# Kernel tuning notes

Measured on AMD Instinct MI355X. Metric: run time of the kernel, lower is better.

The kernel has to match this reference:

```python
import jax, jax.numpy as jnp
import numpy as np

B, L, N, H, D, TOPK = 32, 720, 512, 16, 64, 8
TEMP = 1.0


def setup_inputs() -> dict:
    key = jax.random.key(0)
    ks = jax.random.split(key, 18)
    s = lambda k, shp, fan: jax.random.normal(k, shp, jnp.float32) / np.sqrt(fan)
    return {
        'x': jax.random.normal(ks[0], (B, L, N), jnp.float32),
        'var_embed': s(ks[1], (N, H), H),
        'Wq': s(ks[2], (H, H), H), 'bq': jnp.zeros((H,), jnp.float32),
        'Wk': s(ks[3], (H, H), H), 'bk': jnp.zeros((H,), jnp.float32),
        'Wscore': s(ks[4], (N, 1), N), 'bscore': jnp.zeros((1,), jnp.float32),
        'Wc1': s(ks[5], (N, D), N), 'bc1': jnp.zeros((D,), jnp.float32),
        'Wc2': s(ks[6], (D, D), D), 'bc2': jnp.zeros((D,), jnp.float32),
        'Wcn': s(ks[7], (D, N), D), 'bcn': jnp.zeros((N,), jnp.float32),
        'Wg': s(ks[8], (2 * N, N), 2 * N), 'bg': jnp.zeros((N,), jnp.float32),
        'Wf': s(ks[9], (N, N), N), 'bf': jnp.zeros((N,), jnp.float32),
        'gamma': jnp.ones((N,), jnp.float32), 'beta': jnp.zeros((N,), jnp.float32),
    }


def _forward(x, var_embed, Wq, bq, Wk, bk, Wscore, bscore, Wc1, bc1, Wc2, bc2,
             Wcn, bcn, Wg, bg, Wf, bf, gamma, beta):
    # --- SparseVariableRouter (eval mode: no gumbel noise) ---
    Q = var_embed @ Wq + bq          # [N,H]
    K = var_embed @ Wk + bk          # [N,H]
    sim = Q @ K.T                    # [N,N] (identical across batch in torch)
    eye = jnp.eye(N, dtype=bool)
    sim = jnp.where(eye, -1e9, sim)
    topk_vals, topk_idx = jax.lax.top_k(sim, TOPK)      # [N,k]
    w = jax.nn.softmax(topk_vals / TEMP, axis=-1)        # [N,k]
    x_perm = jnp.transpose(x, (0, 2, 1))                 # [B,N,L]
    neighbors = x_perm[:, topk_idx, :]                   # [B,N,k,L] gather
    ring_out = jnp.einsum('bnkl,nk->bln', neighbors, w)  # [B,L,N]
    # --- center path ---
    attn = jax.nn.softmax(x @ Wscore + bscore, axis=1)   # [B,L,1] softmax over L
    center_raw = jnp.sum(x * attn, axis=1)               # [B,N]
    c = jax.nn.gelu(center_raw @ Wc1 + bc1, approximate=False)
    c = jax.nn.gelu(c @ Wc2 + bc2, approximate=False)
    center = c @ Wcn + bcn                               # [B,N]
    center_b = jnp.broadcast_to(center[:, None, :], (x.shape[0], x.shape[1], N))
    # --- gated fusion + residual LN ---
    gate = jax.nn.sigmoid(jnp.concatenate([ring_out, center_b], axis=-1) @ Wg + bg)
    fused = gate * ring_out + (1.0 - gate) * center_b
    fused = fused @ Wf + bf
    h = fused + x
    mu = jnp.mean(h, axis=-1, keepdims=True)
    var = jnp.var(h, axis=-1, keepdims=True)
    return (h - mu) * jax.lax.rsqrt(var + 1e-5) * gamma + beta


def reference(x, var_embed, Wq, bq, Wk, bk, Wscore, bscore, Wc1, bc1, Wc2, bc2,
              Wcn, bcn, Wg, bg, Wf, bf, gamma, beta):
    return _forward(x, var_embed, Wq, bq, Wk, bk, Wscore, bscore, Wc1, bc1,
                    Wc2, bc2, Wcn, bcn, Wg, bg, Wf, bf, gamma, beta)
```

## Files before the change

### kernel.cpp

```cpp
#include <hip/hip_runtime.h>
#include <hip/hip_bf16.h>
#include <math.h>

#define B_ 32
#define L_ 720
#define N_ 512
#define H_ 16
#define D_ 64
#define TOPK_ 8
#define M_ (B_ * L_)
#define RPB 8
#define CRCH 16
#define CRL (L_ / CRCH)

typedef __bf16 bf16x8 __attribute__((ext_vector_type(8)));
typedef float f32x16 __attribute__((ext_vector_type(16)));

__device__ __forceinline__ void async_cp16(const __hip_bfloat16* g, __hip_bfloat16* l) {
    __builtin_amdgcn_global_load_lds(
        (const __attribute__((address_space(1))) void*)g,
        (__attribute__((address_space(3))) void*)l, 16, 0, 0);
}

__device__ __forceinline__ bf16x8 frag_ld(const __hip_bfloat16* base, int row, int j0) {
    return *(const bf16x8*)(base + row * 64 + (((j0) ^ (row & 7)) << 3));
}

__global__ __launch_bounds__(512) void qk_kernel(
    const float* __restrict__ ve,
    const float* __restrict__ Wq, const float* __restrict__ bq,
    const float* __restrict__ Wk, const float* __restrict__ bk,
    float* __restrict__ Qm, float* __restrict__ Km)
{
    const int g = blockIdx.x * 512 + threadIdx.x;
    const int j = g >> 4, h = g & 15;
    const float* vr = ve + j * H_;
    float q = bq[h], k = bk[h];
    #pragma unroll
    for (int m = 0; m < H_; ++m) {
        const float v = vr[m];
        q += v * Wq[m * H_ + h];
        k += v * Wk[m * H_ + h];
    }
    Qm[g] = q;
    Km[g] = k;
}

__global__ __launch_bounds__(64) void topk_kernel(
    const float* __restrict__ Qm, const float* __restrict__ Km,
    float* __restrict__ w_out, int* __restrict__ idx_out)
{
    const int n = blockIdx.x;
    const int lane = threadIdx.x;

    float4 q0, q1, q2, q3;
    {
        const float4* qr = (const float4*)(Qm + n * H_);
        q0 = qr[0]; q1 = qr[1]; q2 = qr[2]; q3 = qr[3];
    }

    float sv[8]; int si[8];
    #pragma unroll
    for (int c = 0; c < 8; ++c) {
        const int j = c * 64 + lane;
        const float4* kr = (const float4*)(Km + j * H_);
        float4 k0 = kr[0], k1 = kr[1], k2 = kr[2], k3 = kr[3];
        float s = q0.x * k0.x + q0.y * k0.y + q0.z * k0.z + q0.w * k0.w
                + q1.x * k1.x + q1.y * k1.y + q1.z * k1.z + q1.w * k1.w
                + q2.x * k2.x + q2.y * k2.y + q2.z * k2.z + q2.w * k2.w
                + q3.x * k3.x + q3.y * k3.y + q3.z * k3.z + q3.w * k3.w;
        sv[c] = (j == n) ? -1e9f : s;
        si[c] = j;
    }

    float keepv[TOPK_]; int keepi[TOPK_];
    #pragma unroll
    for (int k = 0; k < TOPK_; ++k) {
        float bv = sv[0]; int bi = si[0]; int bslot = 0;
        #pragma unroll
        for (int c = 1; c < 8; ++c)
            if (sv[c] > bv || (sv[c] == bv && si[c] < bi)) { bv = sv[c]; bi = si[c]; bslot = c; }
        float v = bv; int i = bi;
        #pragma unroll
        for (int off = 32; off > 0; off >>= 1) {
            float v2 = __shfl_xor(v, off);
            int   i2 = __shfl_xor(i, off);
            if (v2 > v || (v2 == v && i2 < i)) { v = v2; i = i2; }
        }
        keepv[k] = v; keepi[k] = i;
        if (i == bi) sv[bslot] = -INFINITY;
    }

    if (lane == 0) {
        float vmax = keepv[0];
        float ev[TOPK_], esum = 0.f;
        #pragma unroll
        for (int k = 0; k < TOPK_; k++) { ev[k] = expf(keepv[k] - vmax); esum += ev[k]; }
        float inv = 1.f / esum;
        #pragma unroll
        for (int k = 0; k < TOPK_; k++) {
            w_out[n * TOPK_ + k] = ev[k] * inv;
            idx_out[n * TOPK_ + k] = keepi[k];
        }
    }
}

__global__ __launch_bounds__(512) void ring_kernel(
    const float* __restrict__ x, const float* __restrict__ w,
    const int* __restrict__ idx,
    const float* __restrict__ Wscore, const float* __restrict__ bscore,
    __hip_bfloat16* __restrict__ ring, float* __restrict__ s)
{
    __shared__ float xs[RPB][N_];
    __shared__ float wsh[N_ * TOPK_];
    __shared__ int   ish[N_ * TOPK_];
    const int t = threadIdx.x;
    const int row0 = blockIdx.x * RPB;

    for (int i = t; i < N_ * TOPK_; i += 512) { wsh[i] = w[i]; ish[i] = idx[i]; }
    {
        const float4* xg = (const float4*)(x + (size_t)row0 * N_);
        float4* xsf = (float4*)&xs[0][0];
        xsf[t] = xg[t];
        xsf[t + 512] = xg[t + 512];
    }
    __syncthreads();

    {
        const int wv = t >> 6, lane = t & 63;
        float sa = 0.f;
        #pragma unroll
        for (int i = 0; i < 8; ++i) sa += xs[wv][lane + i * 64] * Wscore[lane + i * 64];
        for (int off = 32; off > 0; off >>= 1) sa += __shfl_down(sa, off);
        if (lane == 0) s[row0 + wv] = sa + bscore[0];
    }

    float wr[TOPK_]; int ir[TOPK_];
    #pragma unroll
    for (int k = 0; k < TOPK_; ++k) { wr[k] = wsh[t * TOPK_ + k]; ir[k] = ish[t * TOPK_ + k]; }
    #pragma unroll
    for (int r = 0; r < RPB; ++r) {
        float acc = 0.f;
        #pragma unroll
        for (int k = 0; k < TOPK_; ++k) acc += wr[k] * xs[r][ir[k]];
        ring[(size_t)(row0 + r) * N_ + t] = __float2bfloat16(acc);
    }
}

__global__ __launch_bounds__(256) void attn_softmax_kernel(float* __restrict__ s)
{
    const int b = blockIdx.x;
    const int t = threadIdx.x;
    float* row = s + (size_t)b * L_;

    __shared__ float sm[4];
    __shared__ float sm2[4];

    float lmax = -1e30f;
    for (int l = t; l < L_; l += 256) lmax = fmaxf(lmax, row[l]);
    for (int off = 32; off > 0; off >>= 1) lmax = fmaxf(lmax, __shfl_down(lmax, off));
    if ((t & 63) == 0) sm[t >> 6] = lmax;
    __syncthreads();
    float gmax = fmaxf(fmaxf(sm[0], sm[1]), fmaxf(sm[2], sm[3]));

    float lsum = 0.f;
    for (int l = t; l < L_; l += 256) {
        float e = expf(row[l] - gmax);
        row[l] = e;
        lsum += e;
    }
    for (int off = 32; off > 0; off >>= 1) lsum += __shfl_down(lsum, off);
    if ((t & 63) == 0) sm2[t >> 6] = lsum;
    __syncthreads();
    float inv = 1.f / (sm2[0] + sm2[1] + sm2[2] + sm2[3]);
    for (int l = t; l < L_; l += 256) row[l] *= inv;
}

__global__ __launch_bounds__(512) void center_raw_kernel(
    const float* __restrict__ x, const float* __restrict__ attn,
    float* __restrict__ craw_p)
{
    const int b = blockIdx.x >> 4;
    const int c = blockIdx.x & 15;
    const int n = threadIdx.x;
    __shared__ float ash[CRL];
    const int l0 = c * CRL;
    if (n < CRL) ash[n] = attn[b * L_ + l0 + n];
    __syncthreads();
    const float* xb = x + ((size_t)b * L_ + l0) * N_;
    float acc = 0.f;
    #pragma unroll 3
    for (int l = 0; l < CRL; l++) acc += ash[l] * xb[(size_t)l * N_ + n];
    craw_p[(size_t)(b * CRCH + c) * N_ + n] = acc;
}

__device__ __forceinline__ float gelu_exact(float v) {
    return 0.5f * v * (1.0f + erff(v * 0.70710678118654752440f));
}

__global__ __launch_bounds__(512) void center_mlp_kernel(
    const float* __restrict__ craw_p,
    const float* __restrict__ Wc1, const float* __restrict__ bc1,
    const float* __restrict__ Wc2, const float* __restrict__ bc2,
    const float* __restrict__ Wcn, const float* __restrict__ bcn,
    float* __restrict__ center)
{
    const int b = blockIdx.x;
    const int t = threadIdx.x;
    const int col = t & 63;
    const int seg = t >> 6;
    __shared__ float cr[N_];
    __shared__ float psum[8][D_];
    __shared__ float h1[D_];
    __shared__ float h2[D_];

    {
        float acc = 0.f;
        #pragma unroll
        for (int c = 0; c < CRCH; ++c) acc += craw_p[(size_t)(b * CRCH + c) * N_ + t];
        cr[t] = acc;
    }
    __syncthreads();
    {
        float p = 0.f;
        #pragma unroll 8
        for (int m = seg * 64; m < seg * 64 + 64; ++m) p += cr[m] * Wc1[m * D_ + col];
        psum[seg][col] = p;
    }
    __syncthreads();
    if (t < D_) {
        float acc = bc1[t];
        #pragma unroll
        for (int s2 = 0; s2 < 8; ++s2) acc += psum[s2][t];
        h1[t] = gelu_exact(acc);
    }
    __syncthreads();
    if (t < D_) {
        float acc = bc2[t];
        #pragma unroll 8
        for (int j = 0; j < D_; j++) acc += h1[j] * Wc2[j * D_ + t];
        h2[t] = gelu_exact(acc);
    }
    __syncthreads();
    {
        float acc = bcn[t];
        #pragma unroll 8
        for (int j = 0; j < D_; j++) acc += h2[j] * Wcn[j * N_ + t];
        center[b * N_ + t] = acc;
    }
}

__global__ __launch_bounds__(512) void cg_kernel(
    const float* __restrict__ center, const float* __restrict__ Wg,
    const float* __restrict__ bg, float* __restrict__ cg)
{
    const int nc = blockIdx.x;
    const int b  = blockIdx.y;
    const int t  = threadIdx.x;
    const int col = nc * 64 + (t & 63);
    const int seg = t >> 6;
    __shared__ float cs[N_];
    __shared__ float psum[8][64];

    cs[t] = center[b * N_ + t];
    __syncthreads();
    {
        float p = 0.f;
        const float* wp = Wg + (size_t)(N_ + seg * 64) * N_ + col;
        #pragma unroll 8
        for (int m = 0; m < 64; ++m) { p += cs[seg * 64 + m] * wp[0]; wp += N_; }
        psum[seg][t & 63] = p;
    }
    __syncthreads();
    if (t < 64) {
        float acc = bg[nc * 64 + t];
        #pragma unroll
        for (int s2 = 0; s2 < 8; ++s2) acc += psum[s2][t];
        cg[b * N_ + nc * 64 + t] = acc;
    }
}

__global__ __launch_bounds__(256) void convert_kernel(
    const float* __restrict__ Wg, const float* __restrict__ Wf,
    __hip_bfloat16* __restrict__ WgT, __hip_bfloat16* __restrict__ WfT)
{
    const int n = blockIdx.x & 511;
    const bool isf = blockIdx.x >= 512;
    const float* src = isf ? Wf : Wg;
    __hip_bfloat16* dst = isf ? WfT : WgT;
    for (int k = threadIdx.x; k < N_; k += 256)
        dst[n * N_ + k] = __float2bfloat16(src[(size_t)k * N_ + n]);
}

#define GEMM_BODY(EPILOGUE)                                                    \
    __shared__ __hip_bfloat16 Ash[128 * 64];                                   \
    __shared__ __hip_bfloat16 Bsh[128 * 64];                                   \
    const int tid  = threadIdx.x;                                              \
    const int lane = tid & 63;                                                 \
    const int wv   = tid >> 6;                                                 \
    const int m32  = lane & 31;                                                \
    const int half = lane >> 5;                                                \
    const int wr   = wv >> 1;                                                  \
    const int wc   = wv & 1;                                                   \
    const int row0 = blockIdx.x * 128;                                         \
    const int n0   = blockIdx.y * 128;                                         \
    const int swz  = (lane & 7) ^ (lane >> 3);                                 \
    const int rln  = lane >> 3;                                                \
    f32x16 acc[2][2];                                                          \
    _Pragma("unroll") for (int i = 0; i < 2; i++)                              \
        _Pragma("unroll") for (int j = 0; j < 2; j++)                          \
            _Pragma("unroll") for (int e = 0; e < 16; e++) acc[i][j][e] = 0.f; \
    for (int step = 0; step < 8; ++step) {                                     \
        const int k0 = step * 64;                                              \
        const __hip_bfloat16* Ab = A  + (size_t)row0 * N_ + k0 + swz * 8;      \
        const __hip_bfloat16* Bb = BT + (size_t)n0   * N_ + k0 + swz * 8;      \
        __syncthreads();                                                       \
        _Pragma("unroll") for (int j = 0; j < 4; ++j) {                        \
            const int r = j * 32 + wv * 8 + rln;                               \
            const int lb = (j * 256 + wv * 64) * 8;                            \
            async_cp16(Ab + (size_t)r * N_, Ash + lb);                         \
            async_cp16(Bb + (size_t)r * N_, Bsh + lb);                         \
        }                                                                      \
        __syncthreads();                                                       \
        _Pragma("unroll") for (int ks = 0; ks < 4; ++ks) {                     \
            const int j0 = ks * 2 + half;                                      \
            bf16x8 a0 = frag_ld(Ash, wr * 64      + m32, j0);                  \
            bf16x8 a1 = frag_ld(Ash, wr * 64 + 32 + m32, j0);                  \
            bf16x8 b0 = frag_ld(Bsh, wc * 64      + m32, j0);                  \
            bf16x8 b1 = frag_ld(Bsh, wc * 64 + 32 + m32, j0);                  \
            acc[0][0] = __builtin_amdgcn_mfma_f32_32x32x16_bf16(a0, b0, acc[0][0], 0, 0, 0); \
            acc[0][1] = __builtin_amdgcn_mfma_f32_32x32x16_bf16(a0, b1, acc[0][1], 0, 0, 0); \
            acc[1][0] = __builtin_amdgcn_mfma_f32_32x32x16_bf16(a1, b0, acc[1][0], 0, 0, 0); \
            acc[1][1] = __builtin_amdgcn_mfma_f32_32x32x16_bf16(a1, b1, acc[1][1], 0, 0, 0); \
        }                                                                      \
    }                                                                          \
    _Pragma("unroll") for (int mi = 0; mi < 2; ++mi)                           \
        _Pragma("unroll") for (int ni = 0; ni < 2; ++ni)                       \
            _Pragma("unroll") for (int reg = 0; reg < 16; ++reg) {             \
                const int rg  = row0 + wr * 64 + mi * 32 +                     \
                                (reg & 3) + 8 * (reg >> 2) + 4 * half;         \
                const int col = n0 + wc * 64 + ni * 32 + m32;                  \
                const float aval = acc[mi][ni][reg];                           \
                EPILOGUE                                                       \
            }

__global__ __launch_bounds__(256) void gemm_gate_kernel(
    const __hip_bfloat16* __restrict__ A,
    const __hip_bfloat16* __restrict__ BT,
    const float* __restrict__ cg,
    const float* __restrict__ center,
    __hip_bfloat16* __restrict__ fused)
{
    GEMM_BODY({
        const int b = rg / L_;
        const float logit = aval + cg[b * N_ + col];
        const float g = 1.f / (1.f + expf(-logit));
        const float rv = __bfloat162float(A[(size_t)rg * N_ + col]);
        const float f = g * rv + (1.f - g) * center[b * N_ + col];
        fused[(size_t)rg * N_ + col] = __float2bfloat16(f);
    })
}

__global__ __launch_bounds__(256) void gemm_out_kernel(
    const __hip_bfloat16* __restrict__ A,
    const __hip_bfloat16* __restrict__ BT,
    const float* __restrict__ x,
    const float* __restrict__ bfv,
    float* __restrict__ out)
{
    GEMM_BODY({
        out[(size_t)rg * N_ + col] = aval + bfv[col] + x[(size_t)rg * N_ + col];
    })
}

__global__ __launch_bounds__(512) void ln_kernel(
    float* __restrict__ out,
    const float* __restrict__ gamma, const float* __restrict__ beta)
{
    const int tid = threadIdx.x;
    const int r = tid >> 7;
    const int c = tid & 127;
    const int row = blockIdx.x * 4 + r;
    const int wid = tid >> 6;
    __shared__ float ls[8], lq[8];

    float4 v = ((const float4*)(out + (size_t)row * N_))[c];
    float sum = v.x + v.y + v.z + v.w;
    float sq  = v.x * v.x + v.y * v.y + v.z * v.z + v.w * v.w;
    for (int off = 32; off > 0; off >>= 1) {
        sum += __shfl_down(sum, off);
        sq  += __shfl_down(sq,  off);
    }
    if ((tid & 63) == 0) { ls[wid] = sum; lq[wid] = sq; }
    __syncthreads();
    const float S  = ls[2 * r] + ls[2 * r + 1];
    const float Q2 = lq[2 * r] + lq[2 * r + 1];
    const float mu  = S * (1.0f / N_);
    const float var = Q2 * (1.0f / N_) - mu * mu;
    const float inv = 1.0f / sqrtf(var + 1e-5f);
    const float4 g4 = ((const float4*)gamma)[c];
    const float4 b4 = ((const float4*)beta)[c];
    float4 o;
    o.x = (v.x - mu) * inv * g4.x + b4.x;
    o.y = (v.y - mu) * inv * g4.y + b4.y;
    o.z = (v.z - mu) * inv * g4.z + b4.z;
    o.w = (v.w - mu) * inv * g4.w + b4.w;
    ((float4*)(out + (size_t)row * N_))[c] = o;
}

extern "C" void kernel_launch(void* const* d_in, const int* in_sizes, int n_in,
                              void* d_out, int out_size, void* d_ws, size_t ws_size,
                              hipStream_t stream) {
    const float* x       = (const float*)d_in[0];
    const float* ve      = (const float*)d_in[1];
    const float* Wq      = (const float*)d_in[2];
    const float* bq      = (const float*)d_in[3];
    const float* Wk      = (const float*)d_in[4];
    const float* bk      = (const float*)d_in[5];
    const float* Wscore  = (const float*)d_in[6];
    const float* bscore  = (const float*)d_in[7];
    const float* Wc1     = (const float*)d_in[8];
    const float* bc1     = (const float*)d_in[9];
    const float* Wc2     = (const float*)d_in[10];
    const float* bc2     = (const float*)d_in[11];
    const float* Wcn     = (const float*)d_in[12];
    const float* bcn     = (const float*)d_in[13];
    const float* Wg      = (const float*)d_in[14];
    const float* bg      = (const float*)d_in[15];
    const float* Wf      = (const float*)d_in[16];
    const float* bf      = (const float*)d_in[17];
    const float* gamma   = (const float*)d_in[18];
    const float* beta    = (const float*)d_in[19];
    float* out = (float*)d_out;

    char* p = (char*)d_ws;
    float* ws_w    = (float*)p; p += N_ * TOPK_ * sizeof(float);
    int*   ws_idx  = (int*)p;   p += N_ * TOPK_ * sizeof(int);
    float* ws_s    = (float*)p; p += B_ * L_ * sizeof(float);
    float* ws_crp  = (float*)p; p += B_ * CRCH * N_ * sizeof(float);
    float* ws_cent = (float*)p; p += B_ * N_ * sizeof(float);
    float* ws_cg   = (float*)p; p += B_ * N_ * sizeof(float);
    float* ws_Q    = (float*)p; p += N_ * H_ * sizeof(float);
    float* ws_K    = (float*)p; p += N_ * H_ * sizeof(float);
    __hip_bfloat16* ws_ring  = (__hip_bfloat16*)p; p += (size_t)M_ * N_ * sizeof(__hip_bfloat16);
    __hip_bfloat16* ws_fused = (__hip_bfloat16*)p; p += (size_t)M_ * N_ * sizeof(__hip_bfloat16);
    __hip_bfloat16* ws_WgT   = (__hip_bfloat16*)p; p += (size_t)N_ * N_ * sizeof(__hip_bfloat16);
    __hip_bfloat16* ws_WfT   = (__hip_bfloat16*)p; p += (size_t)N_ * N_ * sizeof(__hip_bfloat16);

    convert_kernel<<<1024, 256, 0, stream>>>(Wg, Wf, ws_WgT, ws_WfT);
    qk_kernel<<<16, 512, 0, stream>>>(ve, Wq, bq, Wk, bk, ws_Q, ws_K);
    topk_kernel<<<N_, 64, 0, stream>>>(ws_Q, ws_K, ws_w, ws_idx);
    ring_kernel<<<M_ / RPB, 512, 0, stream>>>(x, ws_w, ws_idx, Wscore, bscore,
                                              ws_ring, ws_s);
    attn_softmax_kernel<<<B_, 256, 0, stream>>>(ws_s);
    center_raw_kernel<<<B_ * CRCH, 512, 0, stream>>>(x, ws_s, ws_crp);
    center_mlp_kernel<<<B_, 512, 0, stream>>>(ws_crp, Wc1, bc1, Wc2, bc2,
                                              Wcn, bcn, ws_cent);
    cg_kernel<<<dim3(8, B_), 512, 0, stream>>>(ws_cent, Wg, bg, ws_cg);
    dim3 ggrid(M_ / 128, N_ / 128);
    gemm_gate_kernel<<<ggrid, 256, 0, stream>>>(ws_ring, ws_WgT, ws_cg,
                                                ws_cent, ws_fused);
    gemm_out_kernel<<<ggrid, 256, 0, stream>>>(ws_fused, ws_WfT, x, bf, out);
    ln_kernel<<<M_ / 4, 512, 0, stream>>>(out, gamma, beta);
}
```

Baseline: 268.8 us.

## Fuse gate GEMM, output GEMM and LayerNorm into one row-tile kernel

```diff
diff --git a/kernel.cpp b/kernel.cpp
--- a/kernel.cpp
+++ b/kernel.cpp
@@ -12,6 +12,7 @@
 #define RPB 8
 #define CRCH 16
 #define CRL (L_ / CRCH)
+#define MT 64
 
 typedef __bf16 bf16x8 __attribute__((ext_vector_type(8)));
 typedef float f32x16 __attribute__((ext_vector_type(16)));
@@ -22,28 +23,39 @@
         (__attribute__((address_space(3))) void*)l, 16, 0, 0);
 }
 
-__device__ __forceinline__ bf16x8 frag_ld(const __hip_bfloat16* base, int row, int j0) {
-    return *(const bf16x8*)(base + row * 64 + (((j0) ^ (row & 7)) << 3));
-}
-
-__global__ __launch_bounds__(512) void qk_kernel(
+__device__ __forceinline__ int sw_idx(int row, int col) {
+    return row * 512 + (((col >> 3) ^ (row & 7)) << 3) + (col & 7);
+}
+
+__global__ __launch_bounds__(256) void prep_kernel(
+    const float* __restrict__ Wg, const float* __restrict__ Wf,
+    __hip_bfloat16* __restrict__ WgT, __hip_bfloat16* __restrict__ WfT,
     const float* __restrict__ ve,
     const float* __restrict__ Wq, const float* __restrict__ bq,
     const float* __restrict__ Wk, const float* __restrict__ bk,
     float* __restrict__ Qm, float* __restrict__ Km)
 {
-    const int g = blockIdx.x * 512 + threadIdx.x;
-    const int j = g >> 4, h = g & 15;
-    const float* vr = ve + j * H_;
-    float q = bq[h], k = bk[h];
-    #pragma unroll
-    for (int m = 0; m < H_; ++m) {
-        const float v = vr[m];
-        q += v * Wq[m * H_ + h];
-        k += v * Wk[m * H_ + h];
-    }
-    Qm[g] = q;
-    Km[g] = k;
+    if (blockIdx.x < 1024) {
+        const int n = blockIdx.x & 511;
+        const bool isf = blockIdx.x >= 512;
+        const float* src = isf ? Wf : Wg;
+        __hip_bfloat16* dst = isf ? WfT : WgT;
+        for (int k = threadIdx.x; k < N_; k += 256)
+            dst[n * N_ + k] = __float2bfloat16(src[(size_t)k * N_ + n]);
+    } else {
+        const int g = (blockIdx.x - 1024) * 256 + threadIdx.x;
+        const int j = g >> 4, h = g & 15;
+        const float* vr = ve + j * H_;
+        float q = bq[h], k = bk[h];
+        #pragma unroll
+        for (int m = 0; m < H_; ++m) {
+            const float v = vr[m];
+            q += v * Wq[m * H_ + h];
+            k += v * Wk[m * H_ + h];
+        }
+        Qm[g] = q;
+        Km[g] = k;
+    }
 }
 
 __global__ __launch_bounds__(64) void topk_kernel(
@@ -147,46 +159,40 @@
     }
 }
 
-__global__ __launch_bounds__(256) void attn_softmax_kernel(float* __restrict__ s)
-{
-    const int b = blockIdx.x;
-    const int t = threadIdx.x;
-    float* row = s + (size_t)b * L_;
-
-    __shared__ float sm[4];
-    __shared__ float sm2[4];
-
-    float lmax = -1e30f;
-    for (int l = t; l < L_; l += 256) lmax = fmaxf(lmax, row[l]);
-    for (int off = 32; off > 0; off >>= 1) lmax = fmaxf(lmax, __shfl_down(lmax, off));
-    if ((t & 63) == 0) sm[t >> 6] = lmax;
-    __syncthreads();
-    float gmax = fmaxf(fmaxf(sm[0], sm[1]), fmaxf(sm[2], sm[3]));
-
-    float lsum = 0.f;
-    for (int l = t; l < L_; l += 256) {
-        float e = expf(row[l] - gmax);
-        row[l] = e;
-        lsum += e;
-    }
-    for (int off = 32; off > 0; off >>= 1) lsum += __shfl_down(lsum, off);
-    if ((t & 63) == 0) sm2[t >> 6] = lsum;
-    __syncthreads();
-    float inv = 1.f / (sm2[0] + sm2[1] + sm2[2] + sm2[3]);
-    for (int l = t; l < L_; l += 256) row[l] *= inv;
-}
-
 __global__ __launch_bounds__(512) void center_raw_kernel(
-    const float* __restrict__ x, const float* __restrict__ attn,
+    const float* __restrict__ x, const float* __restrict__ s,
     float* __restrict__ craw_p)
 {
     const int b = blockIdx.x >> 4;
     const int c = blockIdx.x & 15;
     const int n = threadIdx.x;
+    __shared__ float red[8];
     __shared__ float ash[CRL];
+    const float* srow = s + (size_t)b * L_;
+
+    const float v1 = srow[n];
+    const float v2 = (n < L_ - 512) ? srow[512 + n] : -1e30f;
+    float lmax = fmaxf(v1, v2);
+    for (int off = 32; off > 0; off >>= 1) lmax = fmaxf(lmax, __shfl_xor(lmax, off));
+    if ((n & 63) == 0) red[n >> 6] = lmax;
+    __syncthreads();
+    float gmax = red[0];
+    #pragma unroll
+    for (int i = 1; i < 8; ++i) gmax = fmaxf(gmax, red[i]);
+    __syncthreads();
+    float lsum = expf(v1 - gmax) + ((n < L_ - 512) ? expf(v2 - gmax) : 0.f);
+    for (int off = 32; off > 0; off >>= 1) lsum += __shfl_xor(lsum, off);
+    if ((n & 63) == 0) red[n >> 6] = lsum;
+    __syncthreads();
+    float gsum = 0.f;
+    #pragma unroll
+    for (int i = 0; i < 8; ++i) gsum += red[i];
+    const float inv = 1.f / gsum;
+
     const int l0 = c * CRL;
-    if (n < CRL) ash[n] = attn[b * L_ + l0 + n];
-    __syncthreads();
+    if (n < CRL) ash[n] = expf(srow[l0 + n] - gmax) * inv;
+    __syncthreads();
+
     const float* xb = x + ((size_t)b * L_ + l0) * N_;
     float acc = 0.f;
     #pragma unroll 3
@@ -280,132 +286,137 @@
     }
 }
 
-__global__ __launch_bounds__(256) void convert_kernel(
-    const float* __restrict__ Wg, const float* __restrict__ Wf,
-    __hip_bfloat16* __restrict__ WgT, __hip_bfloat16* __restrict__ WfT)
-{
-    const int n = blockIdx.x & 511;
-    const bool isf = blockIdx.x >= 512;
-    const float* src = isf ? Wf : Wg;
-    __hip_bfloat16* dst = isf ? WfT : WgT;
-    for (int k = threadIdx.x; k < N_; k += 256)
-        dst[n * N_ + k] = __float2bfloat16(src[(size_t)k * N_ + n]);
-}
-
-#define GEMM_BODY(EPILOGUE)                                                    \
-    __shared__ __hip_bfloat16 Ash[128 * 64];                                   \
-    __shared__ __hip_bfloat16 Bsh[128 * 64];                                   \
-    const int tid  = threadIdx.x;                                              \
-    const int lane = tid & 63;                                                 \
-    const int wv   = tid >> 6;                                                 \
-    const int m32  = lane & 31;                                                \
-    const int half = lane >> 5;                                                \
-    const int wr   = wv >> 1;                                                  \
-    const int wc   = wv & 1;                                                   \
-    const int row0 = blockIdx.x * 128;                                         \
-    const int n0   = blockIdx.y * 128;                                         \
-    const int swz  = (lane & 7) ^ (lane >> 3);                                 \
-    const int rln  = lane >> 3;                                                \
-    f32x16 acc[2][2];                                                          \
-    _Pragma("unroll") for (int i = 0; i < 2; i++)                              \
-        _Pragma("unroll") for (int j = 0; j < 2; j++)                          \
-            _Pragma("unroll") for (int e = 0; e < 16; e++) acc[i][j][e] = 0.f; \
-    for (int step = 0; step < 8; ++step) {                                     \
-        const int k0 = step * 64;                                              \
-        const __hip_bfloat16* Ab = A  + (size_t)row0 * N_ + k0 + swz * 8;      \
-        const __hip_bfloat16* Bb = BT + (size_t)n0   * N_ + k0 + swz * 8;      \
-        __syncthreads();                                                       \
-        _Pragma("unroll") for (int j = 0; j < 4; ++j) {                        \
-            const int r = j * 32 + wv * 8 + rln;                               \
-            const int lb = (j * 256 + wv * 64) * 8;                            \
-            async_cp16(Ab + (size_t)r * N_, Ash + lb);                         \
-            async_cp16(Bb + (size_t)r * N_, Bsh + lb);                         \
+#define KLOOP(ATILE, BPTR, ACC)                                                \
+    _Pragma("unroll 4")                                                        \
+    for (int ks = 0; ks < 32; ++ks) {                                          \
+        const int arow = wr * 32 + m32;                                        \
+        bf16x8 a = *(const bf16x8*)(ATILE + arow * 512 +                       \
+                      (((2 * ks + half) ^ (arow & 7)) << 3));                  \
+        _Pragma("unroll")                                                      \
+        for (int ni = 0; ni < 4; ++ni) {                                       \
+            const int n = wc * 128 + ni * 32 + m32;                            \
+            bf16x8 b = *(const bf16x8*)(BPTR + (size_t)n * 512 +               \
+                                        ks * 16 + half * 8);                   \
+            ACC[ni] = __builtin_amdgcn_mfma_f32_32x32x16_bf16(a, b, ACC[ni], 0, 0, 0); \
         }                                                                      \
-        __syncthreads();                                                       \
-        _Pragma("unroll") for (int ks = 0; ks < 4; ++ks) {                     \
-            const int j0 = ks * 2 + half;                                      \
-            bf16x8 a0 = frag_ld(Ash, wr * 64      + m32, j0);                  \
-            bf16x8 a1 = frag_ld(Ash, wr * 64 + 32 + m32, j0);                  \
-            bf16x8 b0 = frag_ld(Bsh, wc * 64      + m32, j0);                  \
-            bf16x8 b1 = frag_ld(Bsh, wc * 64 + 32 + m32, j0);                  \
-            acc[0][0] = __builtin_amdgcn_mfma_f32_32x32x16_bf16(a0, b0, acc[0][0], 0, 0, 0); \
-            acc[0][1] = __builtin_amdgcn_mfma_f32_32x32x16_bf16(a0, b1, acc[0][1], 0, 0, 0); \
-            acc[1][0] = __builtin_amdgcn_mfma_f32_32x32x16_bf16(a1, b0, acc[1][0], 0, 0, 0); \
-            acc[1][1] = __builtin_amdgcn_mfma_f32_32x32x16_bf16(a1, b1, acc[1][1], 0, 0, 0); \
-        }                                                                      \
-    }                                                                          \
-    _Pragma("unroll") for (int mi = 0; mi < 2; ++mi)                           \
-        _Pragma("unroll") for (int ni = 0; ni < 2; ++ni)                       \
-            _Pragma("unroll") for (int reg = 0; reg < 16; ++reg) {             \
-                const int rg  = row0 + wr * 64 + mi * 32 +                     \
-                                (reg & 3) + 8 * (reg >> 2) + 4 * half;         \
-                const int col = n0 + wc * 64 + ni * 32 + m32;                  \
-                const float aval = acc[mi][ni][reg];                           \
-                EPILOGUE                                                       \
-            }
-
-__global__ __launch_bounds__(256) void gemm_gate_kernel(
-    const __hip_bfloat16* __restrict__ A,
-    const __hip_bfloat16* __restrict__ BT,
-    const float* __restrict__ cg,
-    const float* __restrict__ center,
-    __hip_bfloat16* __restrict__ fused)
-{
-    GEMM_BODY({
-        const int b = rg / L_;
-        const float logit = aval + cg[b * N_ + col];
-        const float g = 1.f / (1.f + expf(-logit));
-        const float rv = __bfloat162float(A[(size_t)rg * N_ + col]);
-        const float f = g * rv + (1.f - g) * center[b * N_ + col];
-        fused[(size_t)rg * N_ + col] = __float2bfloat16(f);
-    })
-}
-
-__global__ __launch_bounds__(256) void gemm_out_kernel(
-    const __hip_bfloat16* __restrict__ A,
-    const __hip_bfloat16* __restrict__ BT,
-    const float* __restrict__ x,
-    const float* __restrict__ bfv,
+    }
+
+__global__ __launch_bounds__(512, 2) void mega_kernel(
+    const __hip_bfloat16* __restrict__ ring,
+    const __hip_bfloat16* __restrict__ WgT,
+    const __hip_bfloat16* __restrict__ WfT,
+    const float* __restrict__ cg, const float* __restrict__ center,
+    const float* __restrict__ x, const float* __restrict__ bfv,
+    const float* __restrict__ gamma, const float* __restrict__ beta,
     float* __restrict__ out)
 {
-    GEMM_BODY({
-        out[(size_t)rg * N_ + col] = aval + bfv[col] + x[(size_t)rg * N_ + col];
-    })
-}
-
-__global__ __launch_bounds__(512) void ln_kernel(
-    float* __restrict__ out,
-    const float* __restrict__ gamma, const float* __restrict__ beta)
-{
-    const int tid = threadIdx.x;
-    const int r = tid >> 7;
-    const int c = tid & 127;
-    const int row = blockIdx.x * 4 + r;
-    const int wid = tid >> 6;
-    __shared__ float ls[8], lq[8];
-
-    float4 v = ((const float4*)(out + (size_t)row * N_))[c];
-    float sum = v.x + v.y + v.z + v.w;
-    float sq  = v.x * v.x + v.y * v.y + v.z * v.z + v.w * v.w;
-    for (int off = 32; off > 0; off >>= 1) {
-        sum += __shfl_down(sum, off);
-        sq  += __shfl_down(sq,  off);
-    }
-    if ((tid & 63) == 0) { ls[wid] = sum; lq[wid] = sq; }
-    __syncthreads();
-    const float S  = ls[2 * r] + ls[2 * r + 1];
-    const float Q2 = lq[2 * r] + lq[2 * r + 1];
-    const float mu  = S * (1.0f / N_);
-    const float var = Q2 * (1.0f / N_) - mu * mu;
-    const float inv = 1.0f / sqrtf(var + 1e-5f);
-    const float4 g4 = ((const float4*)gamma)[c];
-    const float4 b4 = ((const float4*)beta)[c];
-    float4 o;
-    o.x = (v.x - mu) * inv * g4.x + b4.x;
-    o.y = (v.y - mu) * inv * g4.y + b4.y;
-    o.z = (v.z - mu) * inv * g4.z + b4.z;
-    o.w = (v.w - mu) * inv * g4.w + b4.w;
-    ((float4*)(out + (size_t)row * N_))[c] = o;
+    __shared__ __hip_bfloat16 Ash[MT * 512];
+    const int tid  = threadIdx.x;
+    const int lane = tid & 63;
+    const int wv   = tid >> 6;
+    const int m32  = lane & 31;
+    const int half = lane >> 5;
+    const int wr   = wv >> 2;
+    const int wc   = wv & 3;
+    const int row0 = blockIdx.x * MT;
+
+    #pragma unroll
+    for (int r8 = 0; r8 < 8; ++r8) {
+        const int r = wv * 8 + r8;
+        async_cp16(ring + (size_t)(row0 + r) * N_ + ((lane ^ (r & 7)) << 3),
+                   Ash + r * 512);
+    }
+    __syncthreads();
+
+    f32x16 acc[4];
+    #pragma unroll
+    for (int ni = 0; ni < 4; ++ni)
+        #pragma unroll
+        for (int e = 0; e < 16; ++e) acc[ni][e] = 0.f;
+
+    KLOOP(Ash, WgT, acc)
+    __syncthreads();
+
+    #pragma unroll
+    for (int ni = 0; ni < 4; ++ni) {
+        const int col = wc * 128 + ni * 32 + m32;
+        #pragma unroll
+        for (int reg = 0; reg < 16; ++reg) {
+            const int rl = wr * 32 + (reg & 3) + 8 * (reg >> 2) + 4 * half;
+            const int rg = row0 + rl;
+            const int b  = rg / L_;
+            const float logit = acc[ni][reg] + cg[b * N_ + col];
+            const float g = 1.f / (1.f + expf(-logit));
+            const int ix = sw_idx(rl, col);
+            const float rv = __bfloat162float(Ash[ix]);
+            const float f = g * rv + (1.f - g) * center[b * N_ + col];
+            Ash[ix] = __float2bfloat16(f);
+        }
+    }
+    __syncthreads();
+
+    #pragma unroll
+    for (int ni = 0; ni < 4; ++ni)
+        #pragma unroll
+        for (int e = 0; e < 16; ++e) acc[ni][e] = 0.f;
+
+    KLOOP(Ash, WfT, acc)
+
+    #pragma unroll
+    for (int ni = 0; ni < 4; ++ni) {
+        const int col = wc * 128 + ni * 32 + m32;
+        const float bfc = bfv[col];
+        #pragma unroll
+        for (int reg = 0; reg < 16; ++reg) {
+            const int rl = wr * 32 + (reg & 3) + 8 * (reg >> 2) + 4 * half;
+            acc[ni][reg] += bfc + x[(size_t)(row0 + rl) * N_ + col];
+        }
+    }
+    __syncthreads();
+
+    float* rsum = (float*)Ash;
+    float* rsq  = (float*)Ash + 256;
+    float* muv  = (float*)Ash + 512;
+
+    #pragma unroll
+    for (int reg = 0; reg < 16; ++reg) {
+        float sv = acc[0][reg] + acc[1][reg] + acc[2][reg] + acc[3][reg];
+        float qv = acc[0][reg] * acc[0][reg] + acc[1][reg] * acc[1][reg]
+                 + acc[2][reg] * acc[2][reg] + acc[3][reg] * acc[3][reg];
+        #pragma unroll
+        for (int off = 16; off > 0; off >>= 1) {
+            sv += __shfl_xor(sv, off);
+            qv += __shfl_xor(qv, off);
+        }
+        if (m32 == 0) {
+            const int rl = wr * 32 + (reg & 3) + 8 * (reg >> 2) + 4 * half;
+            rsum[wc * 64 + rl] = sv;
+            rsq [wc * 64 + rl] = qv;
+        }
+    }
+    __syncthreads();
+    if (tid < 64) {
+        const float S = rsum[tid] + rsum[64 + tid] + rsum[128 + tid] + rsum[192 + tid];
+        const float Q = rsq[tid]  + rsq[64 + tid]  + rsq[128 + tid]  + rsq[192 + tid];
+        const float mu  = S * (1.0f / N_);
+        const float var = Q * (1.0f / N_) - mu * mu;
+        muv[tid * 2]     = mu;
+        muv[tid * 2 + 1] = 1.0f / sqrtf(var + 1e-5f);
+    }
+    __syncthreads();
+
+    #pragma unroll
+    for (int ni = 0; ni < 4; ++ni) {
+        const int col = wc * 128 + ni * 32 + m32;
+        const float gm = gamma[col];
+        const float bt = beta[col];
+        #pragma unroll
+        for (int reg = 0; reg < 16; ++reg) {
+            const int rl = wr * 32 + (reg & 3) + 8 * (reg >> 2) + 4 * half;
+            out[(size_t)(row0 + rl) * N_ + col] =
+                (acc[ni][reg] - muv[rl * 2]) * muv[rl * 2 + 1] * gm + bt;
+        }
+    }
 }
 
 extern "C" void kernel_launch(void* const* d_in, const int* in_sizes, int n_in,
@@ -442,24 +453,20 @@
     float* ws_cg   = (float*)p; p += B_ * N_ * sizeof(float);
     float* ws_Q    = (float*)p; p += N_ * H_ * sizeof(float);
     float* ws_K    = (float*)p; p += N_ * H_ * sizeof(float);
-    __hip_bfloat16* ws_ring  = (__hip_bfloat16*)p; p += (size_t)M_ * N_ * sizeof(__hip_bfloat16);
-    __hip_bfloat16* ws_fused = (__hip_bfloat16*)p; p += (size_t)M_ * N_ * sizeof(__hip_bfloat16);
-    __hip_bfloat16* ws_WgT   = (__hip_bfloat16*)p; p += (size_t)N_ * N_ * sizeof(__hip_bfloat16);
-    __hip_bfloat16* ws_WfT   = (__hip_bfloat16*)p; p += (size_t)N_ * N_ * sizeof(__hip_bfloat16);
-
-    convert_kernel<<<1024, 256, 0, stream>>>(Wg, Wf, ws_WgT, ws_WfT);
-    qk_kernel<<<16, 512, 0, stream>>>(ve, Wq, bq, Wk, bk, ws_Q, ws_K);
+    __hip_bfloat16* ws_ring = (__hip_bfloat16*)p; p += (size_t)M_ * N_ * sizeof(__hip_bfloat16);
+    __hip_bfloat16* ws_WgT  = (__hip_bfloat16*)p; p += (size_t)N_ * N_ * sizeof(__hip_bfloat16);
+    __hip_bfloat16* ws_WfT  = (__hip_bfloat16*)p; p += (size_t)N_ * N_ * sizeof(__hip_bfloat16);
+
+    prep_kernel<<<1056, 256, 0, stream>>>(Wg, Wf, ws_WgT, ws_WfT,
+                                          ve, Wq, bq, Wk, bk, ws_Q, ws_K);
     topk_kernel<<<N_, 64, 0, stream>>>(ws_Q, ws_K, ws_w, ws_idx);
     ring_kernel<<<M_ / RPB, 512, 0, stream>>>(x, ws_w, ws_idx, Wscore, bscore,
                                               ws_ring, ws_s);
-    attn_softmax_kernel<<<B_, 256, 0, stream>>>(ws_s);
     center_raw_kernel<<<B_ * CRCH, 512, 0, stream>>>(x, ws_s, ws_crp);
     center_mlp_kernel<<<B_, 512, 0, stream>>>(ws_crp, Wc1, bc1, Wc2, bc2,
                                               Wcn, bcn, ws_cent);
     cg_kernel<<<dim3(8, B_), 512, 0, stream>>>(ws_cent, Wg, bg, ws_cg);
-    dim3 ggrid(M_ / 128, N_ / 128);
-    gemm_gate_kernel<<<ggrid, 256, 0, stream>>>(ws_ring, ws_WgT, ws_cg,
-                                                ws_cent, ws_fused);
-    gemm_out_kernel<<<ggrid, 256, 0, stream>>>(ws_fused, ws_WfT, x, bf, out);
-    ln_kernel<<<M_ / 4, 512, 0, stream>>>(out, gamma, beta);
-}
+    mega_kernel<<<M_ / MT, 512, 0, stream>>>(ws_ring, ws_WgT, ws_WfT,
+                                             ws_cg, ws_cent, x, bf,
+                                             gamma, beta, out);
+}
```

Result: slower. 338.6 us (+26.0%).
